# Kernel tuning notes

Measured on AMD Instinct MI355X. Metric: run time of the kernel, lower is better.

The kernel has to match this reference:

```python
import jax, jax.numpy as jnp
import numpy as np
from jax import lax

# QKeras quantized_bits(8, 0, alpha=1, keep_negative=1):
#   delta = 2^-(bits-1) = 1/128, q(x) = clip(round(x*128), -128, 127)/128
QB_SCALE = 128.0
# QKeras quantized_relu(8, 0): q(x) = clip(round(x*256), 0, 255)/256
QR_SCALE = 256.0

def _ste(q, x):
    # straight-through estimator: forward = q(x), backward = identity
    return x + lax.stop_gradient(q - x)

def qbits(x):
    q = jnp.clip(jnp.round(x * QB_SCALE), -QB_SCALE, QB_SCALE - 1.0) / QB_SCALE
    return _ste(q, x)

def qrelu(x):
    q = jnp.clip(jnp.round(x * QR_SCALE), 0.0, QR_SCALE - 1.0) / QR_SCALE
    return _ste(q, x)


def setup_inputs() -> dict:
    key = jax.random.key(0)
    ks = jax.random.split(key, 9)
    B, C, F = 1000000, 16, 3
    dims = [C * F, 64, 32, 32]
    x = jax.random.normal(ks[0], (B, C, F), dtype=jnp.float32)
    def w(k, i, o):
        return jax.random.normal(k, (i, o), dtype=jnp.float32) * (0.5 / np.sqrt(i))
    inp = {"x": x}
    for li in range(3):
        inp[f"w{li+1}"] = w(ks[1 + 2 * li], dims[li], dims[li + 1])
        inp[f"b{li+1}"] = jax.random.normal(ks[2 + 2 * li], (dims[li + 1],), dtype=jnp.float32) * 0.05
    inp["wout"] = w(ks[7], dims[-1], 5)
    inp["bout"] = jax.random.normal(ks[8], (5,), dtype=jnp.float32) * 0.05
    return inp


def reference(x, w1, b1, w2, b2, w3, b3, wout, bout):
    h = x.reshape(x.shape[0], -1)  # Flatten: [B, 48]
    for w, b in ((w1, b1), (w2, b2), (w3, b3)):
        # QDense: fake-quantize kernel & bias, fp32 matmul, quantized_relu
        h = qrelu(h @ qbits(w) + qbits(b))
    return h @ wout + bout  # final float Dense -> logits [B, 5]
```

## Files before the change

kernel.cpp:

```cpp
#include <hip/hip_runtime.h>
#include <hip/hip_bf16.h>

typedef short  short8 __attribute__((ext_vector_type(8)));
typedef float  f32x4  __attribute__((ext_vector_type(4)));
typedef unsigned int u32;
typedef unsigned long long u64;
typedef unsigned short u16;

__device__ __forceinline__ u32 f2bf(float v) {
    u32 u = __float_as_uint(v);
    return (u + 0x7FFFu + ((u >> 16) & 1u)) >> 16;
}
__device__ __forceinline__ float qround128(float w) {
    float q = rintf(w * 128.0f);
    return fminf(fmaxf(q, -128.0f), 127.0f);
}
__device__ __forceinline__ u32 cvtpk(float a, float b) {
    __hip_bfloat162 h = __float22bfloat162_rn(make_float2(a, b));
    union { __hip_bfloat162 h; u32 u; } cv; cv.h = h; return cv.u;
}
__device__ __forceinline__ u64 qrelu_pack4(f32x4 a) {
    float q0 = fminf(fmaxf(rintf(a[0]), 0.f), 255.f);
    float q1 = fminf(fmaxf(rintf(a[1]), 0.f), 255.f);
    float q2 = fminf(fmaxf(rintf(a[2]), 0.f), 255.f);
    float q3 = fminf(fmaxf(rintf(a[3]), 0.f), 255.f);
    return (u64)cvtpk(q0, q1) | ((u64)cvtpk(q2, q3) << 32);
}
union FragU { short8 s; u32 u[4]; };
__device__ __forceinline__ f32x4 mfma16(short8 a, short8 b, f32x4 c) {
    return __builtin_amdgcn_mfma_f32_16x16x32_bf16(a, b, c, 0, 0, 0);
}

__global__ void prep(const float* __restrict__ w1, const float* __restrict__ b1,
                     const float* __restrict__ w2, const float* __restrict__ b2,
                     const float* __restrict__ w3, const float* __restrict__ b3,
                     const float* __restrict__ wo, const float* __restrict__ bo,
                     u16* __restrict__ wsh) {
    int t = threadIdx.x;
    for (int idx = t; idx < 16 * 512; idx += 256) {
        int blk = idx >> 9, e = idx & 511;
        int l = e >> 3, j = e & 7;
        int r  = l & 15;
        int kk = ((l >> 4) << 3) + j;
        float val = 0.f;
        if (blk < 8) {
            int mt = blk >> 1, ks = blk & 1;
            int k = ks * 32 + kk, fo = mt * 16 + r;
            if (k < 48) val = 2.0f * qround128(w1[k * 64 + fo]);
        } else if (blk < 12) {
            int bi = blk - 8, mt = bi >> 1, ks = bi & 1;
            int k = ks * 32 + kk, fo = mt * 16 + r;
            val = qround128(w2[k * 32 + fo]) * (1.0f / 128.0f);
        } else if (blk < 14) {
            int mt = blk - 12;
            val = qround128(w3[kk * 32 + mt * 16 + r]) * (1.0f / 128.0f);
        } else {
            float wv = (r < 5) ? wo[kk * 5 + r] * (1.0f / 256.0f) : 0.f;
            u32 hb = f2bf(wv);
            if (blk == 14) { wsh[idx] = (u16)hb; continue; }
            val = wv - __uint_as_float(hb << 16);
        }
        wsh[idx] = (u16)f2bf(val);
    }
    float* wsf = (float*)(wsh + 8192);
    for (int i = t; i < 64; i += 256) wsf[i]       = 2.0f * qround128(b1[i]);
    for (int i = t; i < 32; i += 256) wsf[64 + i]  = 2.0f * qround128(b2[i]);
    for (int i = t; i < 32; i += 256) wsf[96 + i]  = 2.0f * qround128(b3[i]);
    for (int i = t; i < 16; i += 256) wsf[128 + i] = (i < 5) ? bo[i] : 0.f;
}


__global__ __launch_bounds__(256, 3) void mlp_mfma(const float* __restrict__ x,
                                                   const u16* __restrict__ wsh,
                                                   float* __restrict__ out, int ntiles) {
    __shared__ __align__(16) u16 smem[4][3840];
    const int tid = threadIdx.x;
    const int wid = tid >> 6, lane = tid & 63;
    const int c = lane & 15, g = lane >> 4;

    short8 wf[16];
    const short8* wv = (const short8*)wsh;
    #pragma unroll
    for (int i = 0; i < 16; ++i) wf[i] = wv[i * 64 + lane];

    const float* wsf = (const float*)(wsh + 8192);
    f32x4 b1q[4], b2q[2], b3q[2], boq;
    #pragma unroll
    for (int i = 0; i < 4; ++i) b1q[i] = *(const f32x4*)(wsf + i * 16 + 4 * g);
    #pragma unroll
    for (int i = 0; i < 2; ++i) b2q[i] = *(const f32x4*)(wsf + 64 + i * 16 + 4 * g);
    #pragma unroll
    for (int i = 0; i < 2; ++i) b3q[i] = *(const f32x4*)(wsf + 96 + i * 16 + 4 * g);
    boq = *(const f32x4*)(wsf + 128 + 4 * g);

    u16* H = &smem[wid][0];
    const int xoff = c * 48 + g * 8;

    const int gw = blockIdx.x * 4 + wid;
    const int nw = gridDim.x * 4;

    for (int t0 = gw; t0 < ntiles; t0 += nw) {
        const float* xl = x + (size_t)t0 * 768 + xoff;
        float4 xa = *(const float4*)(xl);
        float4 xb = *(const float4*)(xl + 4);
        float4 xc = make_float4(0.f, 0.f, 0.f, 0.f);
        float4 xd = make_float4(0.f, 0.f, 0.f, 0.f);
        if (g < 2) { xc = *(const float4*)(xl + 32); xd = *(const float4*)(xl + 36); }

        float v0[8] = {xa.x, xa.y, xa.z, xa.w, xb.x, xb.y, xb.z, xb.w};
        float v1[8] = {xc.x, xc.y, xc.z, xc.w, xd.x, xd.y, xd.z, xd.w};
        FragU bh0, bl0, bh1, bl1;
        #pragma unroll
        for (int p = 0; p < 4; ++p) {
            u32 uu = cvtpk(v0[2 * p], v0[2 * p + 1]);
            bh0.u[p] = uu;
            float r0 = v0[2 * p]     - __uint_as_float(uu << 16);
            float r1 = v0[2 * p + 1] - __uint_as_float(uu & 0xFFFF0000u);
            bl0.u[p] = cvtpk(r0, r1);
            u32 ww = cvtpk(v1[2 * p], v1[2 * p + 1]);
            bh1.u[p] = ww;
            float s0 = v1[2 * p]     - __uint_as_float(ww << 16);
            float s1 = v1[2 * p + 1] - __uint_as_float(ww & 0xFFFF0000u);
            bl1.u[p] = cvtpk(s0, s1);
        }

        #pragma unroll
        for (int mt = 0; mt < 4; ++mt) {
            f32x4 ah = b1q[mt];
            ah = mfma16(wf[mt * 2 + 0], bh0.s, ah);
            ah = mfma16(wf[mt * 2 + 1], bh1.s, ah);
            f32x4 al = {0.f, 0.f, 0.f, 0.f};
            al = mfma16(wf[mt * 2 + 0], bl0.s, al);
            al = mfma16(wf[mt * 2 + 1], bl1.s, al);
            f32x4 a = ah + al;
            *(u64*)(H + c * 80 + mt * 16 + 4 * g) = qrelu_pack4(a);
        }

        short8 p0 = *(const short8*)(H + c * 80 + 8 * g);
        short8 p1 = *(const short8*)(H + c * 80 + 32 + 8 * g);
        #pragma unroll
        for (int mt = 0; mt < 2; ++mt) {
            f32x4 a0 = b2q[mt];
            a0 = mfma16(wf[8 + mt * 2 + 0], p0, a0);
            f32x4 a1 = {0.f, 0.f, 0.f, 0.f};
            a1 = mfma16(wf[8 + mt * 2 + 1], p1, a1);
            f32x4 a = a0 + a1;
            *(u64*)(H + 1280 + c * 80 + mt * 16 + 4 * g) = qrelu_pack4(a);
        }

        short8 p2 = *(const short8*)(H + 1280 + c * 80 + 8 * g);
        #pragma unroll
        for (int mt = 0; mt < 2; ++mt) {
            f32x4 a = b3q[mt];
            a = mfma16(wf[12 + mt], p2, a);
            *(u64*)(H + 2560 + c * 80 + mt * 16 + 4 * g) = qrelu_pack4(a);
        }

        short8 p3 = *(const short8*)(H + 2560 + c * 80 + 8 * g);
        f32x4 aoh = boq;
        aoh = mfma16(wf[14], p3, aoh);
        f32x4 aol = {0.f, 0.f, 0.f, 0.f};
        aol = mfma16(wf[15], p3, aol);
        f32x4 ao = aoh + aol;

        float* orow = out + (size_t)t0 * 80 + c * 5;
        if (g == 0) {
            orow[0] = ao[0]; orow[1] = ao[1]; orow[2] = ao[2]; orow[3] = ao[3];
        } else if (g == 1) {
            orow[4] = ao[0];
        }
    }
}

extern "C" void kernel_launch(void* const* d_in, const int* in_sizes, int n_in,
                              void* d_out, int out_size, void* d_ws, size_t ws_size,
                              hipStream_t stream) {
    const float* x  = (const float*)d_in[0];
    const float* w1 = (const float*)d_in[1];
    const float* b1 = (const float*)d_in[2];
    const float* w2 = (const float*)d_in[3];
    const float* b2 = (const float*)d_in[4];
    const float* w3 = (const float*)d_in[5];
    const float* b3 = (const float*)d_in[6];
    const float* wo = (const float*)d_in[7];
    const float* bo = (const float*)d_in[8];
    float* out = (float*)d_out;

    int B = in_sizes[0] / 48;
    int ntiles = B / 16;

    prep<<<1, 256, 0, stream>>>(w1, b1, w2, b2, w3, b3, wo, bo, (u16*)d_ws);

    int blocks = (ntiles + 3) / 4;
    if (blocks > 2048) blocks = 2048;
    mlp_mfma<<<blocks, 256, 0, stream>>>(x, (const u16*)d_ws, out, ntiles);
}
```

Baseline: 62.70 us.

## Keep MLP activations in registers by permuting weight K-order instead of LDS staging

The weight fragments for layers 2, 3 and the output are permuted in the prep kernel so the MFMA accumulator layout of each layer directly matches the B-operand layout of the next. Activations are then packed in registers rather than written to and read back from shared memory, which removes the LDS round trips and their waits between layers. Launch bounds are loosened from 3 to 2 waves per SIMD, giving more registers at the cost of possibly lower occupancy.

```diff
diff --git a/kernel.cpp b/kernel.cpp
--- a/kernel.cpp
+++ b/kernel.cpp
@@ -19,17 +19,22 @@
     __hip_bfloat162 h = __float22bfloat162_rn(make_float2(a, b));
     union { __hip_bfloat162 h; u32 u; } cv; cv.h = h; return cv.u;
 }
-__device__ __forceinline__ u64 qrelu_pack4(f32x4 a) {
-    float q0 = fminf(fmaxf(rintf(a[0]), 0.f), 255.f);
-    float q1 = fminf(fmaxf(rintf(a[1]), 0.f), 255.f);
-    float q2 = fminf(fmaxf(rintf(a[2]), 0.f), 255.f);
-    float q3 = fminf(fmaxf(rintf(a[3]), 0.f), 255.f);
-    return (u64)cvtpk(q0, q1) | ((u64)cvtpk(q2, q3) << 32);
+__device__ __forceinline__ float q255(float v) {
+    return fminf(fmaxf(rintf(v), 0.f), 255.f);
 }
 union FragU { short8 s; u32 u[4]; };
+__device__ __forceinline__ short8 pack2(f32x4 a, f32x4 b) {
+    FragU f;
+    f.u[0] = cvtpk(q255(a[0]), q255(a[1]));
+    f.u[1] = cvtpk(q255(a[2]), q255(a[3]));
+    f.u[2] = cvtpk(q255(b[0]), q255(b[1]));
+    f.u[3] = cvtpk(q255(b[2]), q255(b[3]));
+    return f.s;
+}
 __device__ __forceinline__ f32x4 mfma16(short8 a, short8 b, f32x4 c) {
     return __builtin_amdgcn_mfma_f32_16x16x32_bf16(a, b, c, 0, 0, 0);
 }
+
 
 __global__ void prep(const float* __restrict__ w1, const float* __restrict__ b1,
                      const float* __restrict__ w2, const float* __restrict__ b2,
@@ -41,7 +46,9 @@
         int blk = idx >> 9, e = idx & 511;
         int l = e >> 3, j = e & 7;
         int r  = l & 15;
-        int kk = ((l >> 4) << 3) + j;
+        int gi = l >> 4;
+        int kk = gi * 8 + j;
+        int fp = 16 * (j >> 2) + 4 * gi + (j & 3);
         float val = 0.f;
         if (blk < 8) {
             int mt = blk >> 1, ks = blk & 1;
@@ -49,13 +56,13 @@
             if (k < 48) val = 2.0f * qround128(w1[k * 64 + fo]);
         } else if (blk < 12) {
             int bi = blk - 8, mt = bi >> 1, ks = bi & 1;
-            int k = ks * 32 + kk, fo = mt * 16 + r;
-            val = qround128(w2[k * 32 + fo]) * (1.0f / 128.0f);
+            int f = ks * 32 + fp, fo = mt * 16 + r;
+            val = qround128(w2[f * 32 + fo]) * (1.0f / 128.0f);
         } else if (blk < 14) {
             int mt = blk - 12;
-            val = qround128(w3[kk * 32 + mt * 16 + r]) * (1.0f / 128.0f);
+            val = qround128(w3[fp * 32 + mt * 16 + r]) * (1.0f / 128.0f);
         } else {
-            float wv = (r < 5) ? wo[kk * 5 + r] * (1.0f / 256.0f) : 0.f;
+            float wv = (r < 5) ? wo[fp * 5 + r] * (1.0f / 256.0f) : 0.f;
             u32 hb = f2bf(wv);
             if (blk == 14) { wsh[idx] = (u16)hb; continue; }
             val = wv - __uint_as_float(hb << 16);
@@ -70,10 +77,9 @@
 }
 
 
-__global__ __launch_bounds__(256, 3) void mlp_mfma(const float* __restrict__ x,
+__global__ __launch_bounds__(256, 2) void mlp_mfma(const float* __restrict__ x,
                                                    const u16* __restrict__ wsh,
                                                    float* __restrict__ out, int ntiles) {
-    __shared__ __align__(16) u16 smem[4][3840];
     const int tid = threadIdx.x;
     const int wid = tid >> 6, lane = tid & 63;
     const int c = lane & 15, g = lane >> 4;
@@ -93,11 +99,10 @@
     for (int i = 0; i < 2; ++i) b3q[i] = *(const f32x4*)(wsf + 96 + i * 16 + 4 * g);
     boq = *(const f32x4*)(wsf + 128 + 4 * g);
 
-    u16* H = &smem[wid][0];
     const int xoff = c * 48 + g * 8;
-
     const int gw = blockIdx.x * 4 + wid;
     const int nw = gridDim.x * 4;
+    const f32x4 zero4 = {0.f, 0.f, 0.f, 0.f};
 
     for (int t0 = gw; t0 < ntiles; t0 += nw) {
         const float* xl = x + (size_t)t0 * 768 + xoff;
@@ -124,43 +129,31 @@
             bl1.u[p] = cvtpk(s0, s1);
         }
 
+        f32x4 acc1[4];
         #pragma unroll
         for (int mt = 0; mt < 4; ++mt) {
-            f32x4 ah = b1q[mt];
-            ah = mfma16(wf[mt * 2 + 0], bh0.s, ah);
+            f32x4 ah = mfma16(wf[mt * 2 + 0], bh0.s, b1q[mt]);
             ah = mfma16(wf[mt * 2 + 1], bh1.s, ah);
-            f32x4 al = {0.f, 0.f, 0.f, 0.f};
-            al = mfma16(wf[mt * 2 + 0], bl0.s, al);
+            f32x4 al = mfma16(wf[mt * 2 + 0], bl0.s, zero4);
             al = mfma16(wf[mt * 2 + 1], bl1.s, al);
-            f32x4 a = ah + al;
-            *(u64*)(H + c * 80 + mt * 16 + 4 * g) = qrelu_pack4(a);
+            acc1[mt] = ah + al;
         }
 
-        short8 p0 = *(const short8*)(H + c * 80 + 8 * g);
-        short8 p1 = *(const short8*)(H + c * 80 + 32 + 8 * g);
-        #pragma unroll
-        for (int mt = 0; mt < 2; ++mt) {
-            f32x4 a0 = b2q[mt];
-            a0 = mfma16(wf[8 + mt * 2 + 0], p0, a0);
-            f32x4 a1 = {0.f, 0.f, 0.f, 0.f};
-            a1 = mfma16(wf[8 + mt * 2 + 1], p1, a1);
-            f32x4 a = a0 + a1;
-            *(u64*)(H + 1280 + c * 80 + mt * 16 + 4 * g) = qrelu_pack4(a);
-        }
+        short8 p0 = pack2(acc1[0], acc1[1]);
+        short8 p1 = pack2(acc1[2], acc1[3]);
 
-        short8 p2 = *(const short8*)(H + 1280 + c * 80 + 8 * g);
-        #pragma unroll
-        for (int mt = 0; mt < 2; ++mt) {
-            f32x4 a = b3q[mt];
-            a = mfma16(wf[12 + mt], p2, a);
-            *(u64*)(H + 2560 + c * 80 + mt * 16 + 4 * g) = qrelu_pack4(a);
-        }
+        f32x4 a20 = mfma16(wf[8],  p0, b2q[0]);
+        f32x4 a21 = mfma16(wf[9],  p1, zero4);
+        f32x4 a22 = mfma16(wf[10], p0, b2q[1]);
+        f32x4 a23 = mfma16(wf[11], p1, zero4);
+        short8 p2 = pack2(a20 + a21, a22 + a23);
 
-        short8 p3 = *(const short8*)(H + 2560 + c * 80 + 8 * g);
-        f32x4 aoh = boq;
-        aoh = mfma16(wf[14], p3, aoh);
-        f32x4 aol = {0.f, 0.f, 0.f, 0.f};
-        aol = mfma16(wf[15], p3, aol);
+        f32x4 a30 = mfma16(wf[12], p2, b3q[0]);
+        f32x4 a31 = mfma16(wf[13], p2, b3q[1]);
+        short8 p3 = pack2(a30, a31);
+
+        f32x4 aoh = mfma16(wf[14], p3, boq);
+        f32x4 aol = mfma16(wf[15], p3, zero4);
         f32x4 ao = aoh + aol;
 
         float* orow = out + (size_t)t0 * 80 + c * 5;
```

Result: faster. 59.10 us (-5.7%).
